# Kernel optimization log

Hardware: AMD Instinct MI355X
Metric: run time of the kernel (lower is better)

## Reference

```python
import jax, jax.numpy as jnp
import numpy as np

B, N_VEC, N_DIM, N_W, N_HID, VOCAB, N_CLASS = 16, 2048, 32, 4, 128, 32000, 10


def setup_inputs() -> dict:
    key = jax.random.key(0)
    ks = jax.random.split(key, 8)
    data = jax.random.randint(ks[0], (B, N_VEC), 0, VOCAB, dtype=jnp.int64)
    emb = jax.random.normal(ks[1], (VOCAB, N_DIM), dtype=jnp.float32) * 0.1
    # stacked per-layer weights for the n_W WModules: Linear(n_dim->n_hid), GELU, Linear(n_hid->n_vec)
    fw1 = jax.random.normal(ks[2], (N_W, N_DIM, N_HID), dtype=jnp.float32) * (1.0 / np.sqrt(N_DIM))
    fb1 = jnp.zeros((N_W, N_HID), dtype=jnp.float32)
    fw2 = jax.random.normal(ks[3], (N_W, N_HID, N_VEC), dtype=jnp.float32) * (1.0 / np.sqrt(N_HID))
    fb2 = jnp.zeros((N_W, N_VEC), dtype=jnp.float32)
    Wf = jax.random.normal(ks[4], (N_VEC * N_DIM, N_CLASS), dtype=jnp.float32) * (1.0 / np.sqrt(N_VEC * N_DIM))
    bf = jnp.zeros((N_CLASS,), dtype=jnp.float32)
    return {"data": data, "emb": emb, "fw1": fw1, "fb1": fb1, "fw2": fw2, "fb2": fb2, "Wf": Wf, "bf": bf}


def reference(data, emb, fw1, fb1, fw2, fb2, Wf, bf):
    X = emb[data]                       # [B, n_vec, n_dim]
    V = X                               # g is identity (with_g=False)
    # iterate over self.fs[::-1]: indices n_W-1 .. 0
    for i in range(N_W - 1, -1, -1):
        h = jax.nn.gelu(jnp.einsum('bnd,dh->bnh', X, fw1[i]) + fb1[i], approximate=False)
        W = jnp.einsum('bnh,hm->bnm', h, fw2[i]) + fb2[i]   # [B, n_vec, n_vec]
        V = jnp.einsum('bnm,bmd->bnd', W, V)                # [B, n_vec, n_dim]
    out = V.reshape(V.shape[0], -1) @ Wf + bf               # [B, n_class]
    return out
```

## Files before the change

### kernel.cpp

```cpp
#include <hip/hip_runtime.h>

#define NB 16
#define NVEC 2048
#define NDIM 32
#define NW 4
#define NHID 128
#define NCLASS 10
#define TPSZ (129 * 132)
#define TP4  (TPSZ / 4)
#define USZ  (129 * 32)
#define U4   (USZ / 4)

__device__ __forceinline__ float gelu_fast(float x) {
    float t = 1.5957691216057308f * x * (1.0f + 0.044715f * x * x);
    return x / (1.0f + __expf(-t));
}

__global__ __launch_bounds__(256, 1) void k_big(const int* __restrict__ data,
                                                const float* __restrict__ emb,
                                                const float* __restrict__ fw1,
                                                const float* __restrict__ fb1,
                                                const float* __restrict__ fw2,
                                                const float* __restrict__ fb2,
                                                float* __restrict__ X,
                                                float* __restrict__ Tpart,
                                                float* __restrict__ U3part) {
    __shared__ float hbuf[128 * 132];
    __shared__ float ws[128 * 132];
    __shared__ float fb2s[128];
    int tid = threadIdx.x, bx = blockIdx.x;

    if (bx < 256) {
        int b = bx >> 4, chunk = bx & 15, m0 = chunk * 128;
        const float* fw2l = fw2 + 3 * (size_t)NHID * NVEC;
        float* xs = hbuf;
#pragma unroll
        for (int jj = 0; jj < 4; ++jj) {
            int i4 = tid + jj * 256;
            int r = i4 >> 3, c4 = (i4 & 7) * 4;
            int idx = data[b * NVEC + m0 + r];
            float4 v = *(const float4*)&emb[(size_t)idx * NDIM + c4];
            *(float4*)&xs[r * 36 + c4] = v;
            *(float4*)&X[((size_t)b * NVEC + m0 + r) * NDIM + c4] = v;
        }
        if (tid < 128) fb2s[tid] = fb2[3 * NVEC + m0 + tid];
        __syncthreads();
        int kg = tid & 31, d0 = (tid >> 5) * 4;
        float acc[4][4];
#pragma unroll
        for (int i = 0; i < 4; ++i)
#pragma unroll
            for (int q = 0; q < 4; ++q) acc[i][q] = 0.f;
        for (int mm = 0; mm < 128; mm += 4) {
            float4 w[4], v[4];
#pragma unroll
            for (int i = 0; i < 4; ++i)
                w[i] = *(const float4*)&fw2l[(size_t)(kg + 32 * i) * NVEC + m0 + mm];
#pragma unroll
            for (int q = 0; q < 4; ++q)
                v[q] = *(const float4*)&xs[(mm + q) * 36 + d0];
#pragma unroll
            for (int i = 0; i < 4; ++i) {
                const float* wf = (const float*)&w[i];
#pragma unroll
                for (int q = 0; q < 4; ++q) {
                    float wv = wf[q];
                    acc[i][0] += wv * v[q].x; acc[i][1] += wv * v[q].y;
                    acc[i][2] += wv * v[q].z; acc[i][3] += wv * v[q].w;
                }
            }
        }
        float* Up = U3part + (size_t)(b * 16 + chunk) * USZ;
#pragma unroll
        for (int i = 0; i < 4; ++i)
            *(float4*)&Up[(kg + 32 * i) * 32 + d0] =
                make_float4(acc[i][0], acc[i][1], acc[i][2], acc[i][3]);
        if (tid < 32) {
            float ca = 0.f;
#pragma unroll 8
            for (int mm = 0; mm < 128; ++mm) ca += fb2s[mm] * xs[mm * 36 + tid];
            Up[128 * 32 + tid] = ca;
        }
    } else {
        int t = bx - 256;
        int j = t >> 8, rr = t & 255;
        int b = rr >> 4, chunk = rr & 15, m0 = chunk * 128;
        const float* w1l  = fw1 + (size_t)(j + 1) * NDIM * NHID;
        const float* b1l  = fb1 + (size_t)(j + 1) * NHID;
        const float* fw2l = fw2 + (size_t)j * NHID * NVEC;
        float* xs  = hbuf;
        float* w1s = hbuf + 128 * 33;
#pragma unroll
        for (int jj = 0; jj < 4; ++jj) {
            int i4 = tid + jj * 256;
            int r = i4 >> 3, c4 = (i4 & 7) * 4;
            int idx = data[b * NVEC + m0 + r];
            float4 v = *(const float4*)&emb[(size_t)idx * NDIM + c4];
            xs[r * 33 + c4] = v.x; xs[r * 33 + c4 + 1] = v.y;
            xs[r * 33 + c4 + 2] = v.z; xs[r * 33 + c4 + 3] = v.w;
        }
#pragma unroll
        for (int jj = 0; jj < 4; ++jj) {
            int i4 = tid + jj * 256;
            int d = i4 >> 5, c4 = (i4 & 31) * 4;
            *(float4*)&w1s[d * 132 + c4] = *(const float4*)&w1l[d * NHID + c4];
        }
#pragma unroll
        for (int jj = 0; jj < 16; ++jj) {
            int i4 = tid + jj * 256;
            int p = i4 >> 5, c4 = (i4 & 31) * 4;
            *(float4*)&ws[p * 132 + c4] =
                *(const float4*)&fw2l[(size_t)p * NVEC + m0 + c4];
        }
        if (tid < 128) fb2s[tid] = fb2[(size_t)j * NVEC + m0 + tid];
        __syncthreads();

        int rg = tid & 31, kg = tid >> 5, k0 = kg * 16;
        float hr[4][16];
        {
            float4 bq[4];
#pragma unroll
            for (int q = 0; q < 4; ++q) bq[q] = *(const float4*)&b1l[k0 + 4 * q];
#pragma unroll
            for (int i = 0; i < 4; ++i)
#pragma unroll
                for (int q = 0; q < 4; ++q) {
                    hr[i][4 * q]     = bq[q].x; hr[i][4 * q + 1] = bq[q].y;
                    hr[i][4 * q + 2] = bq[q].z; hr[i][4 * q + 3] = bq[q].w;
                }
        }
#pragma unroll 4
        for (int d = 0; d < NDIM; ++d) {
            float xv[4];
#pragma unroll
            for (int i = 0; i < 4; ++i) xv[i] = xs[(rg + 32 * i) * 33 + d];
            const float* wrow = &w1s[d * 132 + k0];
            float4 w0 = *(const float4*)wrow;
            float4 w1 = *(const float4*)(wrow + 4);
            float4 w2 = *(const float4*)(wrow + 8);
            float4 w3 = *(const float4*)(wrow + 12);
            float wk[16] = {w0.x, w0.y, w0.z, w0.w, w1.x, w1.y, w1.z, w1.w,
                            w2.x, w2.y, w2.z, w2.w, w3.x, w3.y, w3.z, w3.w};
#pragma unroll
            for (int i = 0; i < 4; ++i)
#pragma unroll
                for (int q = 0; q < 16; ++q) hr[i][q] += xv[i] * wk[q];
        }
        __syncthreads();
#pragma unroll
        for (int i = 0; i < 4; ++i) {
            int row = rg + 32 * i;
#pragma unroll
            for (int q4 = 0; q4 < 4; ++q4) {
                float4 o;
                o.x = gelu_fast(hr[i][4 * q4]);     o.y = gelu_fast(hr[i][4 * q4 + 1]);
                o.z = gelu_fast(hr[i][4 * q4 + 2]); o.w = gelu_fast(hr[i][4 * q4 + 3]);
                *(float4*)&hbuf[row * 132 + k0 + 4 * q4] = o;
            }
            if (kg == 0) hbuf[row * 132 + 128] = 1.0f;
        }
        __syncthreads();

        {
            int pg = tid & 15, q0 = (tid >> 4) * 8;
            float acc[8][8];
#pragma unroll
            for (int i = 0; i < 8; ++i)
#pragma unroll
                for (int q = 0; q < 8; ++q) acc[i][q] = 0.f;
            for (int mt = 0; mt < 128; mt += 4) {
                float4 wv4[8];
#pragma unroll
                for (int i = 0; i < 8; ++i)
                    wv4[i] = *(const float4*)&ws[(pg + 16 * i) * 132 + mt];
                float4 ha[4], hb[4];
#pragma unroll
                for (int mm = 0; mm < 4; ++mm) {
                    ha[mm] = *(const float4*)&hbuf[(mt + mm) * 132 + q0];
                    hb[mm] = *(const float4*)&hbuf[(mt + mm) * 132 + q0 + 4];
                }
#pragma unroll
                for (int i = 0; i < 8; ++i) {
                    const float* wf = (const float*)&wv4[i];
#pragma unroll
                    for (int mm = 0; mm < 4; ++mm) {
                        float w = wf[mm];
                        acc[i][0] += w * ha[mm].x; acc[i][1] += w * ha[mm].y;
                        acc[i][2] += w * ha[mm].z; acc[i][3] += w * ha[mm].w;
                        acc[i][4] += w * hb[mm].x; acc[i][5] += w * hb[mm].y;
                        acc[i][6] += w * hb[mm].z; acc[i][7] += w * hb[mm].w;
                    }
                }
            }
            float* Tp = Tpart + (size_t)t * TPSZ;
#pragma unroll
            for (int i = 0; i < 8; ++i) {
                *(float4*)&Tp[(pg + 16 * i) * 132 + q0] =
                    make_float4(acc[i][0], acc[i][1], acc[i][2], acc[i][3]);
                *(float4*)&Tp[(pg + 16 * i) * 132 + q0 + 4] =
                    make_float4(acc[i][4], acc[i][5], acc[i][6], acc[i][7]);
            }
        }
        if (tid < 128) {
            float s = 0.f;
            const float* wb = &fw2l[(size_t)tid * NVEC + m0];
#pragma unroll 8
            for (int mm = 0; mm < 128; mm += 4) {
                float4 wq = *(const float4*)&wb[mm];
                s += wq.x + wq.y + wq.z + wq.w;
            }
            Tpart[(size_t)t * TPSZ + tid * 132 + 128] = s;
        }
        if (tid < 129) {
            float s = 0.f;
#pragma unroll 8
            for (int mm = 0; mm < 128; ++mm) s += fb2s[mm] * hbuf[mm * 132 + tid];
            Tpart[(size_t)t * TPSZ + 128 * 132 + tid] = s;
        }
    }
}

__global__ __launch_bounds__(256) void k_red(const float* __restrict__ Tpart,
                                             const float* __restrict__ U3part,
                                             float* __restrict__ Tfin,
                                             float* __restrict__ U3fin) {
    int x = blockIdx.x, y = blockIdx.y, tid = threadIdx.x;
    if (y < 48) {
        int i4 = x * 256 + tid;
        if (i4 >= TP4) return;
        float4 s = ((const float4*)Tpart)[(size_t)(y * 16) * TP4 + i4];
#pragma unroll
        for (int c = 1; c < 16; ++c) {
            float4 v = ((const float4*)Tpart)[(size_t)(y * 16 + c) * TP4 + i4];
            s.x += v.x; s.y += v.y; s.z += v.z; s.w += v.w;
        }
        ((float4*)Tfin)[(size_t)y * TP4 + i4] = s;
    } else {
        int b = y - 48;
        int i4 = x * 256 + tid;
        if (i4 >= U4) return;
        float4 s = ((const float4*)U3part)[(size_t)(b * 16) * U4 + i4];
#pragma unroll
        for (int c = 1; c < 16; ++c) {
            float4 v = ((const float4*)U3part)[(size_t)(b * 16 + c) * U4 + i4];
            s.x += v.x; s.y += v.y; s.z += v.z; s.w += v.w;
        }
        ((float4*)U3fin)[(size_t)b * U4 + i4] = s;
    }
}

__global__ __launch_bounds__(256) void k_chain(const float* __restrict__ Tfin,
                                               const float* __restrict__ U3fin,
                                               const float* __restrict__ bf,
                                               float* __restrict__ U0,
                                               float* __restrict__ out) {
    __shared__ float Ul[2][129 * 4];
    int dg = blockIdx.x, b = blockIdx.y, tid = threadIdx.x;
    int d0 = dg * 4;
    if (dg == 0 && tid < NCLASS) out[b * NCLASS + tid] = bf[tid];
    if (tid < 129)
        *(float4*)&Ul[0][tid * 4] =
            *(const float4*)&U3fin[(size_t)b * USZ + tid * 32 + d0];
    int cur = 0;
    float4 acc = make_float4(0.f, 0.f, 0.f, 0.f);
    for (int j = 2; j >= 0; --j) {
        __syncthreads();
        if (tid < 129) {
            const float* rowp = Tfin + (size_t)(j * 16 + b) * TPSZ + tid * 132;
            acc = make_float4(0.f, 0.f, 0.f, 0.f);
            for (int r4 = 0; r4 < 32; ++r4) {
                float4 tv = *(const float4*)&rowp[4 * r4];
                float4 u0 = *(const float4*)&Ul[cur][(4 * r4 + 0) * 4];
                float4 u1 = *(const float4*)&Ul[cur][(4 * r4 + 1) * 4];
                float4 u2 = *(const float4*)&Ul[cur][(4 * r4 + 2) * 4];
                float4 u3 = *(const float4*)&Ul[cur][(4 * r4 + 3) * 4];
                acc.x += tv.x * u0.x + tv.y * u1.x + tv.z * u2.x + tv.w * u3.x;
                acc.y += tv.x * u0.y + tv.y * u1.y + tv.z * u2.y + tv.w * u3.y;
                acc.z += tv.x * u0.z + tv.y * u1.z + tv.z * u2.z + tv.w * u3.z;
                acc.w += tv.x * u0.w + tv.y * u1.w + tv.z * u2.w + tv.w * u3.w;
            }
            float tl = rowp[128];
            float4 ub = *(const float4*)&Ul[cur][128 * 4];
            acc.x += tl * ub.x; acc.y += tl * ub.y;
            acc.z += tl * ub.z; acc.w += tl * ub.w;
        }
        __syncthreads();
        if (tid < 129) *(float4*)&Ul[cur ^ 1][tid * 4] = acc;
        cur ^= 1;
    }
    if (tid < 129)
        *(float4*)&U0[(size_t)b * USZ + tid * 32 + d0] = acc;
}

__global__ __launch_bounds__(256) void k_final(const float* __restrict__ X,
                                               const float* __restrict__ fw1,
                                               const float* __restrict__ fb1,
                                               const float* __restrict__ U0,
                                               const float* __restrict__ Wf,
                                               float* __restrict__ out) {
    __shared__ float xs[64 * 36];
    __shared__ float w1s[32 * 132];
    __shared__ float hs[64 * 132];
    __shared__ float Us[USZ];
    __shared__ float ored[4][NCLASS];
    int ng = blockIdx.x, b = blockIdx.y, tid = threadIdx.x;
    int n0 = ng * 64;
#pragma unroll
    for (int jj = 0; jj < 2; ++jj) {
        int i4 = tid + jj * 256;
        int r = i4 >> 3, c4 = (i4 & 7) * 4;
        *(float4*)&xs[r * 36 + c4] =
            *(const float4*)&X[((size_t)b * NVEC + n0 + r) * NDIM + c4];
    }
#pragma unroll
    for (int jj = 0; jj < 4; ++jj) {
        int i4 = tid + jj * 256;
        int d = i4 >> 5, c4 = (i4 & 31) * 4;
        *(float4*)&w1s[d * 132 + c4] = *(const float4*)&fw1[d * NHID + c4];
    }
    for (int i4 = tid; i4 < U4; i4 += 256)
        ((float4*)Us)[i4] = ((const float4*)(U0 + (size_t)b * USZ))[i4];
    __syncthreads();

    int rg = tid & 31;
    {
        int k0 = (tid >> 5) * 16;
        float acc[2][16];
        {
            float4 bq[4];
#pragma unroll
            for (int q = 0; q < 4; ++q) bq[q] = *(const float4*)&fb1[k0 + 4 * q];
#pragma unroll
            for (int q = 0; q < 4; ++q) {
                acc[0][4 * q] = bq[q].x; acc[0][4 * q + 1] = bq[q].y;
                acc[0][4 * q + 2] = bq[q].z; acc[0][4 * q + 3] = bq[q].w;
                acc[1][4 * q] = bq[q].x; acc[1][4 * q + 1] = bq[q].y;
                acc[1][4 * q + 2] = bq[q].z; acc[1][4 * q + 3] = bq[q].w;
            }
        }
#pragma unroll 4
        for (int d = 0; d < NDIM; ++d) {
            float x0 = xs[rg * 36 + d];
            float x1 = xs[(rg + 32) * 36 + d];
            const float* wrow = &w1s[d * 132 + k0];
            float4 w0 = *(const float4*)wrow;
            float4 w1 = *(const float4*)(wrow + 4);
            float4 w2 = *(const float4*)(wrow + 8);
            float4 w3 = *(const float4*)(wrow + 12);
            float wk[16] = {w0.x, w0.y, w0.z, w0.w, w1.x, w1.y, w1.z, w1.w,
                            w2.x, w2.y, w2.z, w2.w, w3.x, w3.y, w3.z, w3.w};
#pragma unroll
            for (int q = 0; q < 16; ++q) {
                acc[0][q] += x0 * wk[q];
                acc[1][q] += x1 * wk[q];
            }
        }
#pragma unroll
        for (int r = 0; r < 2; ++r) {
            int row = rg + 32 * r;
#pragma unroll
            for (int q4 = 0; q4 < 4; ++q4) {
                float4 o;
                o.x = gelu_fast(acc[r][4 * q4]);     o.y = gelu_fast(acc[r][4 * q4 + 1]);
                o.z = gelu_fast(acc[r][4 * q4 + 2]); o.w = gelu_fast(acc[r][4 * q4 + 3]);
                *(float4*)&hs[row * 132 + k0 + 4 * q4] = o;
            }
        }
    }
    __syncthreads();

    int dg = (tid >> 5) & 3, kh = tid >> 7;
    int d0 = dg * 8, kb = kh * 64;
    float a[2][8];
#pragma unroll
    for (int r = 0; r < 2; ++r)
#pragma unroll
        for (int q = 0; q < 8; ++q) a[r][q] = 0.f;
#pragma unroll 4
    for (int ks = 0; ks < 64; ks += 4) {
        int kk = kb + ks;
        float4 h0 = *(const float4*)&hs[rg * 132 + kk];
        float4 h1 = *(const float4*)&hs[(rg + 32) * 132 + kk];
        float4 u[4][2];
#pragma unroll
        for (int q = 0; q < 4; ++q) {
            u[q][0] = *(const float4*)&Us[(kk + q) * 32 + d0];
            u[q][1] = *(const float4*)&Us[(kk + q) * 32 + d0 + 4];
        }
        const float* hf0 = (const float*)&h0;
        const float* hf1 = (const float*)&h1;
#pragma unroll
        for (int q = 0; q < 4; ++q) {
            float v0 = hf0[q], v1 = hf1[q];
            a[0][0] += v0 * u[q][0].x; a[0][1] += v0 * u[q][0].y;
            a[0][2] += v0 * u[q][0].z; a[0][3] += v0 * u[q][0].w;
            a[0][4] += v0 * u[q][1].x; a[0][5] += v0 * u[q][1].y;
            a[0][6] += v0 * u[q][1].z; a[0][7] += v0 * u[q][1].w;
            a[1][0] += v1 * u[q][0].x; a[1][1] += v1 * u[q][0].y;
            a[1][2] += v1 * u[q][0].z; a[1][3] += v1 * u[q][0].w;
            a[1][4] += v1 * u[q][1].x; a[1][5] += v1 * u[q][1].y;
            a[1][6] += v1 * u[q][1].z; a[1][7] += v1 * u[q][1].w;
        }
    }
    if (kh == 1) {
#pragma unroll
        for (int r = 0; r < 2; ++r) {
            float* p = &xs[(rg + 32 * r) * 36 + d0];
            *(float4*)p       = make_float4(a[r][0], a[r][1], a[r][2], a[r][3]);
            *(float4*)(p + 4) = make_float4(a[r][4], a[r][5], a[r][6], a[r][7]);
        }
    }
    __syncthreads();
    float accC[NCLASS];
#pragma unroll
    for (int c = 0; c < NCLASS; ++c) accC[c] = 0.f;
    if (kh == 0) {
        float4 ub0 = *(const float4*)&Us[128 * 32 + d0];
        float4 ub1 = *(const float4*)&Us[128 * 32 + d0 + 4];
#pragma unroll
        for (int r = 0; r < 2; ++r) {
            const float* p = &xs[(rg + 32 * r) * 36 + d0];
            float4 p0 = *(const float4*)p;
            float4 p1 = *(const float4*)(p + 4);
            a[r][0] += p0.x + ub0.x; a[r][1] += p0.y + ub0.y;
            a[r][2] += p0.z + ub0.z; a[r][3] += p0.w + ub0.w;
            a[r][4] += p1.x + ub1.x; a[r][5] += p1.y + ub1.y;
            a[r][6] += p1.z + ub1.z; a[r][7] += p1.w + ub1.w;
            int nrow = n0 + rg + 32 * r;
#pragma unroll
            for (int dd = 0; dd < 8; ++dd) {
                float v = a[r][dd];
                const float2* wr =
                    (const float2*)(Wf + ((size_t)nrow * 32 + d0 + dd) * NCLASS);
#pragma unroll
                for (int p5 = 0; p5 < 5; ++p5) {
                    float2 w = wr[p5];
                    accC[2 * p5]     += v * w.x;
                    accC[2 * p5 + 1] += v * w.y;
                }
            }
        }
    }
#pragma unroll
    for (int c = 0; c < NCLASS; ++c)
#pragma unroll
        for (int off = 32; off >= 1; off >>= 1)
            accC[c] += __shfl_down(accC[c], off, 64);
    int w = tid >> 6;
    if ((tid & 63) == 0) {
#pragma unroll
        for (int c = 0; c < NCLASS; ++c) ored[w][c] = accC[c];
    }
    __syncthreads();
    if (tid < NCLASS)
        atomicAdd(&out[b * NCLASS + tid],
                  ored[0][tid] + ored[1][tid] + ored[2][tid] + ored[3][tid]);
}

extern "C" void kernel_launch(void* const* d_in, const int* in_sizes, int n_in,
                              void* d_out, int out_size, void* d_ws, size_t ws_size,
                              hipStream_t stream) {
    const int*   data = (const int*)d_in[0];
    const float* emb  = (const float*)d_in[1];
    const float* fw1  = (const float*)d_in[2];
    const float* fb1  = (const float*)d_in[3];
    const float* fw2  = (const float*)d_in[4];
    const float* fb2  = (const float*)d_in[5];
    const float* Wf   = (const float*)d_in[6];
    const float* bf   = (const float*)d_in[7];
    float* out = (float*)d_out;

    float* X      = (float*)d_ws;
    float* Tpart  = X + (size_t)NB * NVEC * NDIM;
    float* U3part = Tpart + (size_t)768 * TPSZ;
    float* Tfin   = U3part + (size_t)256 * USZ;
    float* U3fin  = Tfin + (size_t)48 * TPSZ;
    float* U0     = U3fin + (size_t)NB * USZ;

    k_big<<<1024, 256, 0, stream>>>(data, emb, fw1, fb1, fw2, fb2, X, Tpart, U3part);
    k_red<<<dim3(17, 64), 256, 0, stream>>>(Tpart, U3part, Tfin, U3fin);
    k_chain<<<dim3(8, NB), 256, 0, stream>>>(Tfin, U3fin, bf, U0, out);
    k_final<<<dim3(32, NB), 256, 0, stream>>>(X, fw1, fb1, U0, Wf, out);
}
```

Before: 202.6 us.

## Double k_big block size to 512 threads with split-K reduction in LDS

k_big now launches 512 threads per block and distributes work across the extra threads. In the T-part GEMM, the 128-long reduction is split into two halves, and the two partial sums are combined through shared memory before the write. The weight row-sum is now read from the shared-memory tile instead of global memory. The aim is more waves per CU and less per-thread register pressure, which should hide latency better. The cost is extra barriers and an LDS round trip for the partial-sum combine, and shared memory use (~135KB per block) may still limit residency to one block per CU.

```diff
diff --git a/kernel.cpp b/kernel.cpp
--- a/kernel.cpp
+++ b/kernel.cpp
@@ -16,7 +16,7 @@
     return x / (1.0f + __expf(-t));
 }
 
-__global__ __launch_bounds__(256, 1) void k_big(const int* __restrict__ data,
+__global__ __launch_bounds__(512, 2) void k_big(const int* __restrict__ data,
                                                 const float* __restrict__ emb,
                                                 const float* __restrict__ fw1,
                                                 const float* __restrict__ fb1,
@@ -35,8 +35,8 @@
         const float* fw2l = fw2 + 3 * (size_t)NHID * NVEC;
         float* xs = hbuf;
 #pragma unroll
-        for (int jj = 0; jj < 4; ++jj) {
-            int i4 = tid + jj * 256;
+        for (int jj = 0; jj < 2; ++jj) {
+            int i4 = tid + jj * 512;
             int r = i4 >> 3, c4 = (i4 & 7) * 4;
             int idx = data[b * NVEC + m0 + r];
             float4 v = *(const float4*)&emb[(size_t)idx * NDIM + c4];
@@ -45,22 +45,22 @@
         }
         if (tid < 128) fb2s[tid] = fb2[3 * NVEC + m0 + tid];
         __syncthreads();
-        int kg = tid & 31, d0 = (tid >> 5) * 4;
-        float acc[4][4];
-#pragma unroll
-        for (int i = 0; i < 4; ++i)
+        int kg = tid & 63, d0 = (tid >> 6) * 4;
+        float acc[2][4];
+#pragma unroll
+        for (int i = 0; i < 2; ++i)
 #pragma unroll
             for (int q = 0; q < 4; ++q) acc[i][q] = 0.f;
         for (int mm = 0; mm < 128; mm += 4) {
-            float4 w[4], v[4];
-#pragma unroll
-            for (int i = 0; i < 4; ++i)
-                w[i] = *(const float4*)&fw2l[(size_t)(kg + 32 * i) * NVEC + m0 + mm];
+            float4 w[2], v[4];
+#pragma unroll
+            for (int i = 0; i < 2; ++i)
+                w[i] = *(const float4*)&fw2l[(size_t)(kg + 64 * i) * NVEC + m0 + mm];
 #pragma unroll
             for (int q = 0; q < 4; ++q)
                 v[q] = *(const float4*)&xs[(mm + q) * 36 + d0];
 #pragma unroll
-            for (int i = 0; i < 4; ++i) {
+            for (int i = 0; i < 2; ++i) {
                 const float* wf = (const float*)&w[i];
 #pragma unroll
                 for (int q = 0; q < 4; ++q) {
@@ -72,8 +72,8 @@
         }
         float* Up = U3part + (size_t)(b * 16 + chunk) * USZ;
 #pragma unroll
-        for (int i = 0; i < 4; ++i)
-            *(float4*)&Up[(kg + 32 * i) * 32 + d0] =
+        for (int i = 0; i < 2; ++i)
+            *(float4*)&Up[(kg + 64 * i) * 32 + d0] =
                 make_float4(acc[i][0], acc[i][1], acc[i][2], acc[i][3]);
         if (tid < 32) {
             float ca = 0.f;
@@ -91,8 +91,8 @@
         float* xs  = hbuf;
         float* w1s = hbuf + 128 * 33;
 #pragma unroll
-        for (int jj = 0; jj < 4; ++jj) {
-            int i4 = tid + jj * 256;
+        for (int jj = 0; jj < 2; ++jj) {
+            int i4 = tid + jj * 512;
             int r = i4 >> 3, c4 = (i4 & 7) * 4;
             int idx = data[b * NVEC + m0 + r];
             float4 v = *(const float4*)&emb[(size_t)idx * NDIM + c4];
@@ -100,14 +100,14 @@
             xs[r * 33 + c4 + 2] = v.z; xs[r * 33 + c4 + 3] = v.w;
         }
 #pragma unroll
-        for (int jj = 0; jj < 4; ++jj) {
-            int i4 = tid + jj * 256;
+        for (int jj = 0; jj < 2; ++jj) {
+            int i4 = tid + jj * 512;
             int d = i4 >> 5, c4 = (i4 & 31) * 4;
             *(float4*)&w1s[d * 132 + c4] = *(const float4*)&w1l[d * NHID + c4];
         }
 #pragma unroll
-        for (int jj = 0; jj < 16; ++jj) {
-            int i4 = tid + jj * 256;
+        for (int jj = 0; jj < 8; ++jj) {
+            int i4 = tid + jj * 512;
             int p = i4 >> 5, c4 = (i4 & 31) * 4;
             *(float4*)&ws[p * 132 + c4] =
                 *(const float4*)&fw2l[(size_t)p * NVEC + m0 + c4];
@@ -115,108 +115,117 @@
         if (tid < 128) fb2s[tid] = fb2[(size_t)j * NVEC + m0 + tid];
         __syncthreads();
 
-        int rg = tid & 31, kg = tid >> 5, k0 = kg * 16;
-        float hr[4][16];
+        int rg = tid & 31, kg = tid >> 5, k0 = kg * 8;
         {
-            float4 bq[4];
-#pragma unroll
-            for (int q = 0; q < 4; ++q) bq[q] = *(const float4*)&b1l[k0 + 4 * q];
+            float hr[4][8];
+            float4 b0 = *(const float4*)&b1l[k0];
+            float4 b1v = *(const float4*)&b1l[k0 + 4];
+            float bk[8] = {b0.x, b0.y, b0.z, b0.w, b1v.x, b1v.y, b1v.z, b1v.w};
 #pragma unroll
             for (int i = 0; i < 4; ++i)
 #pragma unroll
-                for (int q = 0; q < 4; ++q) {
-                    hr[i][4 * q]     = bq[q].x; hr[i][4 * q + 1] = bq[q].y;
-                    hr[i][4 * q + 2] = bq[q].z; hr[i][4 * q + 3] = bq[q].w;
+                for (int q = 0; q < 8; ++q) hr[i][q] = bk[q];
+#pragma unroll 4
+            for (int d = 0; d < NDIM; ++d) {
+                float xv[4];
+#pragma unroll
+                for (int i = 0; i < 4; ++i) xv[i] = xs[(rg + 32 * i) * 33 + d];
+                const float* wrow = &w1s[d * 132 + k0];
+                float4 w0 = *(const float4*)wrow;
+                float4 w1 = *(const float4*)(wrow + 4);
+                float wk[8] = {w0.x, w0.y, w0.z, w0.w, w1.x, w1.y, w1.z, w1.w};
+#pragma unroll
+                for (int i = 0; i < 4; ++i)
+#pragma unroll
+                    for (int q = 0; q < 8; ++q) hr[i][q] += xv[i] * wk[q];
+            }
+            __syncthreads();
+#pragma unroll
+            for (int i = 0; i < 4; ++i) {
+                int row = rg + 32 * i;
+                float4 o0, o1;
+                o0.x = gelu_fast(hr[i][0]); o0.y = gelu_fast(hr[i][1]);
+                o0.z = gelu_fast(hr[i][2]); o0.w = gelu_fast(hr[i][3]);
+                o1.x = gelu_fast(hr[i][4]); o1.y = gelu_fast(hr[i][5]);
+                o1.z = gelu_fast(hr[i][6]); o1.w = gelu_fast(hr[i][7]);
+                *(float4*)&hbuf[row * 132 + k0]     = o0;
+                *(float4*)&hbuf[row * 132 + k0 + 4] = o1;
+                if (kg == 0) hbuf[row * 132 + 128] = 1.0f;
+            }
+        }
+        __syncthreads();
+
+        int pg = tid & 15, qg = (tid >> 4) & 15, mh = tid >> 8;
+        int q0 = qg * 8, mbase = mh * 64;
+        float acc[8][8];
+#pragma unroll
+        for (int i = 0; i < 8; ++i)
+#pragma unroll
+            for (int q = 0; q < 8; ++q) acc[i][q] = 0.f;
+        for (int mt = mbase; mt < mbase + 64; mt += 4) {
+            float4 wv4[8];
+#pragma unroll
+            for (int i = 0; i < 8; ++i)
+                wv4[i] = *(const float4*)&ws[(pg + 16 * i) * 132 + mt];
+            float4 ha[4], hb[4];
+#pragma unroll
+            for (int mm = 0; mm < 4; ++mm) {
+                ha[mm] = *(const float4*)&hbuf[(mt + mm) * 132 + q0];
+                hb[mm] = *(const float4*)&hbuf[(mt + mm) * 132 + q0 + 4];
+            }
+#pragma unroll
+            for (int i = 0; i < 8; ++i) {
+                const float* wf = (const float*)&wv4[i];
+#pragma unroll
+                for (int mm = 0; mm < 4; ++mm) {
+                    float w = wf[mm];
+                    acc[i][0] += w * ha[mm].x; acc[i][1] += w * ha[mm].y;
+                    acc[i][2] += w * ha[mm].z; acc[i][3] += w * ha[mm].w;
+                    acc[i][4] += w * hb[mm].x; acc[i][5] += w * hb[mm].y;
+                    acc[i][6] += w * hb[mm].z; acc[i][7] += w * hb[mm].w;
                 }
-        }
-#pragma unroll 4
-        for (int d = 0; d < NDIM; ++d) {
-            float xv[4];
-#pragma unroll
-            for (int i = 0; i < 4; ++i) xv[i] = xs[(rg + 32 * i) * 33 + d];
-            const float* wrow = &w1s[d * 132 + k0];
-            float4 w0 = *(const float4*)wrow;
-            float4 w1 = *(const float4*)(wrow + 4);
-            float4 w2 = *(const float4*)(wrow + 8);
-            float4 w3 = *(const float4*)(wrow + 12);
-            float wk[16] = {w0.x, w0.y, w0.z, w0.w, w1.x, w1.y, w1.z, w1.w,
-                            w2.x, w2.y, w2.z, w2.w, w3.x, w3.y, w3.z, w3.w};
-#pragma unroll
-            for (int i = 0; i < 4; ++i)
-#pragma unroll
-                for (int q = 0; q < 16; ++q) hr[i][q] += xv[i] * wk[q];
-        }
-        __syncthreads();
-#pragma unroll
-        for (int i = 0; i < 4; ++i) {
-            int row = rg + 32 * i;
-#pragma unroll
-            for (int q4 = 0; q4 < 4; ++q4) {
-                float4 o;
-                o.x = gelu_fast(hr[i][4 * q4]);     o.y = gelu_fast(hr[i][4 * q4 + 1]);
-                o.z = gelu_fast(hr[i][4 * q4 + 2]); o.w = gelu_fast(hr[i][4 * q4 + 3]);
-                *(float4*)&hbuf[row * 132 + k0 + 4 * q4] = o;
-            }
-            if (kg == 0) hbuf[row * 132 + 128] = 1.0f;
-        }
-        __syncthreads();
-
-        {
-            int pg = tid & 15, q0 = (tid >> 4) * 8;
-            float acc[8][8];
-#pragma unroll
-            for (int i = 0; i < 8; ++i)
-#pragma unroll
-                for (int q = 0; q < 8; ++q) acc[i][q] = 0.f;
-            for (int mt = 0; mt < 128; mt += 4) {
-                float4 wv4[8];
-#pragma unroll
-                for (int i = 0; i < 8; ++i)
-                    wv4[i] = *(const float4*)&ws[(pg + 16 * i) * 132 + mt];
-                float4 ha[4], hb[4];
-#pragma unroll
-                for (int mm = 0; mm < 4; ++mm) {
-                    ha[mm] = *(const float4*)&hbuf[(mt + mm) * 132 + q0];
-                    hb[mm] = *(const float4*)&hbuf[(mt + mm) * 132 + q0 + 4];
-                }
-#pragma unroll
-                for (int i = 0; i < 8; ++i) {
-                    const float* wf = (const float*)&wv4[i];
-#pragma unroll
-                    for (int mm = 0; mm < 4; ++mm) {
-                        float w = wf[mm];
-                        acc[i][0] += w * ha[mm].x; acc[i][1] += w * ha[mm].y;
-                        acc[i][2] += w * ha[mm].z; acc[i][3] += w * ha[mm].w;
-                        acc[i][4] += w * hb[mm].x; acc[i][5] += w * hb[mm].y;
-                        acc[i][6] += w * hb[mm].z; acc[i][7] += w * hb[mm].w;
-                    }
-                }
-            }
-            float* Tp = Tpart + (size_t)t * TPSZ;
+            }
+        }
+        __syncthreads();
+
+        float scol = 0.f, brow = 0.f;
+        if (tid < 128) {
+#pragma unroll 8
+            for (int mm = 0; mm < 128; ++mm) scol += ws[tid * 132 + mm];
+        }
+        if (tid < 129) {
+#pragma unroll 8
+            for (int mm = 0; mm < 128; ++mm) brow += fb2s[mm] * hbuf[mm * 132 + tid];
+        }
+        __syncthreads();
+
+        if (mh == 1) {
 #pragma unroll
             for (int i = 0; i < 8; ++i) {
+                *(float4*)&ws[(pg + 16 * i) * 132 + q0] =
+                    make_float4(acc[i][0], acc[i][1], acc[i][2], acc[i][3]);
+                *(float4*)&ws[(pg + 16 * i) * 132 + q0 + 4] =
+                    make_float4(acc[i][4], acc[i][5], acc[i][6], acc[i][7]);
+            }
+        }
+        __syncthreads();
+
+        float* Tp = Tpart + (size_t)t * TPSZ;
+        if (mh == 0) {
+#pragma unroll
+            for (int i = 0; i < 8; ++i) {
+                float4 p0 = *(const float4*)&ws[(pg + 16 * i) * 132 + q0];
+                float4 p1 = *(const float4*)&ws[(pg + 16 * i) * 132 + q0 + 4];
                 *(float4*)&Tp[(pg + 16 * i) * 132 + q0] =
-                    make_float4(acc[i][0], acc[i][1], acc[i][2], acc[i][3]);
+                    make_float4(acc[i][0] + p0.x, acc[i][1] + p0.y,
+                                acc[i][2] + p0.z, acc[i][3] + p0.w);
                 *(float4*)&Tp[(pg + 16 * i) * 132 + q0 + 4] =
-                    make_float4(acc[i][4], acc[i][5], acc[i][6], acc[i][7]);
-            }
-        }
-        if (tid < 128) {
-            float s = 0.f;
-            const float* wb = &fw2l[(size_t)tid * NVEC + m0];
-#pragma unroll 8
-            for (int mm = 0; mm < 128; mm += 4) {
-                float4 wq = *(const float4*)&wb[mm];
-                s += wq.x + wq.y + wq.z + wq.w;
-            }
-            Tpart[(size_t)t * TPSZ + tid * 132 + 128] = s;
-        }
-        if (tid < 129) {
-            float s = 0.f;
-#pragma unroll 8
-            for (int mm = 0; mm < 128; ++mm) s += fb2s[mm] * hbuf[mm * 132 + tid];
-            Tpart[(size_t)t * TPSZ + 128 * 132 + tid] = s;
-        }
+                    make_float4(acc[i][4] + p1.x, acc[i][5] + p1.y,
+                                acc[i][6] + p1.z, acc[i][7] + p1.w);
+            }
+        }
+        if (tid < 128) Tp[tid * 132 + 128] = scol;
+        if (tid < 129) Tp[128 * 132 + tid] = brow;
     }
 }
 
@@ -477,7 +486,7 @@
     float* U3fin  = Tfin + (size_t)48 * TPSZ;
     float* U0     = U3fin + (size_t)NB * USZ;
 
-    k_big<<<1024, 256, 0, stream>>>(data, emb, fw1, fb1, fw2, fb2, X, Tpart, U3part);
+    k_big<<<1024, 512, 0, stream>>>(data, emb, fw1, fb1, fw2, fb2, X, Tpart, U3part);
     k_red<<<dim3(17, 64), 256, 0, stream>>>(Tpart, U3part, Tfin, U3fin);
     k_chain<<<dim3(8, NB), 256, 0, stream>>>(Tfin, U3fin, bf, U0, out);
     k_final<<<dim3(32, NB), 256, 0, stream>>>(X, fw1, fb1, U0, Wf, out);
```

Measured after the change: 196.2 us. -3.1%, faster.
